# Optimization experiments

Hardware: AMD Instinct MI355X
Metric: run time of the kernel (lower is better)

Reference implementation:

```python
import jax, jax.numpy as jnp
import numpy as np

N = 100000
E = 1600000
NFEAT, NHID, NCLASS = 128, 64, 40
EPS = 1e-5


def _sage_conv(x, src, dst, wl, wr, b):
    # mean aggregation over in-neighbors: out[dst] = mean_{src->dst} x[src]
    msg = jax.ops.segment_sum(x[src], dst, num_segments=N)          # [N, d]
    deg = jax.ops.segment_sum(jnp.ones((src.shape[0],), x.dtype), dst, num_segments=N)
    agg = msg / jnp.maximum(deg, 1.0)[:, None]
    return agg @ wl + x @ wr + b


def _bn_eval(x, g, b, m, v):
    return (x - m) * (g * jax.lax.rsqrt(v + EPS)) + b


def setup_inputs() -> dict:
    key = jax.random.key(0)
    ks = jax.random.split(key, 12)
    s = 0.05
    x = jax.random.normal(ks[0], (N, NFEAT), dtype=jnp.float32)
    edge_index = jax.random.randint(ks[1], (2, E), 0, N, dtype=jnp.int64)
    inp = {
        'x': x,
        'edge_index': edge_index,
        'w1l': jax.random.normal(ks[2], (NFEAT, NHID), jnp.float32) * s,
        'w1r': jax.random.normal(ks[3], (NFEAT, NHID), jnp.float32) * s,
        'b1': jnp.zeros((NHID,), jnp.float32),
        'wxl': jax.random.normal(ks[4], (NHID, NHID), jnp.float32) * s,
        'wxr': jax.random.normal(ks[5], (NHID, NHID), jnp.float32) * s,
        'bx': jnp.zeros((NHID,), jnp.float32),
        'w2l': jax.random.normal(ks[6], (NHID, NCLASS), jnp.float32) * s,
        'w2r': jax.random.normal(ks[7], (NHID, NCLASS), jnp.float32) * s,
        'b2': jnp.zeros((NCLASS,), jnp.float32),
        'bn3_g': jnp.ones((NHID,), jnp.float32),
        'bn3_b': jnp.zeros((NHID,), jnp.float32),
        'bn3_m': jax.random.normal(ks[8], (NHID,), jnp.float32) * 0.1,
        'bn3_v': jax.random.uniform(ks[9], (NHID,), jnp.float32, 0.5, 1.5),
        'bn2_g': jnp.ones((NCLASS,), jnp.float32),
        'bn2_b': jnp.zeros((NCLASS,), jnp.float32),
        'bn2_m': jax.random.normal(ks[10], (NCLASS,), jnp.float32) * 0.1,
        'bn2_v': jax.random.uniform(ks[11], (NCLASS,), jnp.float32, 0.5, 1.5),
    }
    return inp


def reference(x, edge_index, w1l, w1r, b1, wxl, wxr, bx, w2l, w2r, b2,
              bn3_g, bn3_b, bn3_m, bn3_v, bn2_g, bn2_b, bn2_m, bn2_v):
    src, dst = edge_index[0], edge_index[1]
    h = jax.nn.relu(_sage_conv(x, src, dst, w1l, w1r, b1))          # conv1 + relu
    # middle layer (layer=3 -> one convx iteration); dropout = identity (eval)
    h = _sage_conv(h, src, dst, wxl, wxr, bx)
    h = jax.nn.relu(_bn_eval(h, bn3_g, bn3_b, bn3_m, bn3_v))
    # final layer
    h = _sage_conv(h, src, dst, w2l, w2r, b2)
    return _bn_eval(h, bn2_g, bn2_b, bn2_m, bn2_v)                  # [N, NCLASS]
```

## Files before the change

kernel.cpp:

```cpp
#include <hip/hip_runtime.h>

#define NNODES 100000
#define NEDGES 1600000
#define NBK    196
#define BK_CAP 9000
#define CHUNK  4096

typedef short bhalf8 __attribute__((ext_vector_type(8)));
typedef float f32x4 __attribute__((ext_vector_type(4)));

__device__ __forceinline__ unsigned fbits(float x){ union{float f;unsigned u;}c; c.f=x; return c.u; }
__device__ __forceinline__ float bcast(unsigned u){ union{float f;unsigned u;}c; c.u=u; return c.f; }
__device__ __forceinline__ unsigned short rtn16(float x){
    unsigned u = fbits(x);
    return (unsigned short)((u + 0x7FFFu + ((u >> 16) & 1u)) >> 16);
}
__device__ __forceinline__ float b2f(unsigned short b){ return bcast((unsigned)b << 16); }

__global__ void detect_kernel(const int* __restrict__ ei, int* __restrict__ flag) {
    int t = threadIdx.x;
    int v = ei[2 * t + 1];
    unsigned long long nz = __ballot(v != 0);
    if (t == 0) flag[0] = (nz == 0ULL) ? 1 : 0;
}

__global__ __launch_bounds__(256) void bucketize(
    const int* __restrict__ ei, const int* __restrict__ flag,
    unsigned* __restrict__ recs, int* __restrict__ bcur) {
    const int is64 = flag[0];
    __shared__ int cnt[256], base[256], loc[256], rnk[256];
    __shared__ unsigned stage[CHUNK];
    __shared__ unsigned char bkof[CHUNK];
    const int t = threadIdx.x;
    const long start = (long)blockIdx.x * CHUNK;
    cnt[t] = 0; rnk[t] = 0;
    __syncthreads();
#pragma unroll
    for (int k = 0; k < CHUNK / 256; ++k) {
        long e = start + k * 256 + t;
        if (e < NEDGES) {
            int d = is64 ? ei[2 * (NEDGES + e)] : ei[NEDGES + e];
            atomicAdd(&cnt[d >> 9], 1);
        }
    }
    __syncthreads();
    int v = cnt[t];
    int run = v;
    loc[t] = run;
    __syncthreads();
    for (int off = 1; off < 256; off <<= 1) {
        int other = (t >= off) ? loc[t - off] : 0;
        __syncthreads();
        run += other;
        loc[t] = run;
        __syncthreads();
    }
    int excl = run - v;
    if (v > 0) base[t] = atomicAdd(&bcur[t], v);
    loc[t] = excl;
    __syncthreads();
#pragma unroll
    for (int k = 0; k < CHUNK / 256; ++k) {
        long e = start + k * 256 + t;
        if (e < NEDGES) {
            int s = is64 ? ei[2 * e] : ei[e];
            int d = is64 ? ei[2 * (NEDGES + e)] : ei[NEDGES + e];
            int b = d >> 9;
            int r = atomicAdd(&rnk[b], 1);
            int pos = loc[b] + r;
            stage[pos] = ((unsigned)s << 9) | (unsigned)(d & 511);
            bkof[pos] = (unsigned char)b;
        }
    }
    __syncthreads();
    const int tot = (int)min((long)CHUNK, NEDGES - start);
    for (int i = t; i < tot; i += 256) {
        int b = bkof[i];
        int pos = base[b] + (i - loc[b]);
        if (pos < BK_CAP)
            recs[(size_t)b * BK_CAP + pos] = stage[i];
    }
}

__global__ __launch_bounds__(512) void csr_build(
    const unsigned* __restrict__ recs, const int* __restrict__ bcur,
    int* __restrict__ offs, int* __restrict__ csr) {
    const int b = blockIdx.x;
    const int t = threadIdx.x;
    const int lo = b << 9;
    __shared__ int sc[512];
    __shared__ int hist[512];
    __shared__ int loff[512];
    int bv = (t < NBK) ? bcur[t] : 0;
    int run = bv;
    sc[t] = run;
    __syncthreads();
    for (int off = 1; off < 512; off <<= 1) {
        int other = (t >= off) ? sc[t - off] : 0;
        __syncthreads();
        run += other;
        sc[t] = run;
        __syncthreads();
    }
    const int n = bcur[b];
    const int csr_base = sc[b] - n;
    const unsigned* P = recs + (size_t)b * BK_CAP;
    hist[t] = 0;
    __syncthreads();
    for (int i = t; i < n; i += 512)
        atomicAdd(&hist[P[i] & 511], 1);
    __syncthreads();
    int hv = hist[t];
    int hrun = hv;
    sc[t] = hrun;
    __syncthreads();
    for (int off = 1; off < 512; off <<= 1) {
        int other = (t >= off) ? sc[t - off] : 0;
        __syncthreads();
        hrun += other;
        sc[t] = hrun;
        __syncthreads();
    }
    int ex = hrun - hv;
    loff[t] = ex;
    int node = lo + t;
    if (node < NNODES) offs[node] = csr_base + ex;
    if (b == NBK - 1 && t == 0) offs[NNODES] = NEDGES;
    __syncthreads();
    hist[t] = loff[t];
    __syncthreads();
    for (int i = t; i < n; i += 512) {
        unsigned rec = P[i];
        int r = atomicAdd(&hist[rec & 511], 1);
        csr[csr_base + r] = (int)(rec >> 9) * 128;
    }
}

template <int K, int NL, int NTOT>
__global__ void prep_w(const float* __restrict__ wl, const float* __restrict__ wr,
                       const float* __restrict__ bias,
                       const float* __restrict__ g, const float* __restrict__ bb,
                       const float* __restrict__ m, const float* __restrict__ vv,
                       unsigned short* __restrict__ Bh, unsigned short* __restrict__ Bl,
                       float* __restrict__ bfix) {
    constexpr int NCT = NTOT / 16;
    constexpr int TOT = (K / 32) * NCT * 512;
    int tid = blockIdx.x * blockDim.x + threadIdx.x;
    if (tid < NL) {
        float sc = g ? g[tid] * rsqrtf(vv[tid] + 1e-5f) : 1.f;
        float sh = g ? (bb[tid] - m[tid] * sc) : 0.f;
        bfix[tid] = bias[tid] * sc + sh;
    }
    for (int idx = tid; idx < TOT; idx += gridDim.x * blockDim.x) {
        int e = idx & 7, l = (idx >> 3) & 63, rest = idx >> 9;
        int ct = rest % NCT, kc = rest / NCT;
        int k = kc * 32 + (l >> 4) * 8 + e;
        int j = ct * 16 + (l & 15);
        int jj = (j < NL) ? j : j - NL;
        float sc = g ? g[jj] * rsqrtf(vv[jj] + 1e-5f) : 1.f;
        float v = ((j < NL) ? wl[k * NL + j] : wr[k * NL + (j - NL)]) * sc;
        unsigned short h = rtn16(v);
        float r1 = v - bcast((unsigned)h << 16);
        Bh[idx] = h;
        Bl[idx] = rtn16(r1);
    }
}

template <int K, int NL, int NTOT, bool ABF16>
__global__ __launch_bounds__(256) void gemm_mfma(
    const void* __restrict__ hvp, const unsigned short* __restrict__ Bh,
    const unsigned short* __restrict__ Bl, const float* __restrict__ bias,
    unsigned short* __restrict__ zl, unsigned short* __restrict__ zr, int nrows) {
    constexpr int NCT = NTOT / 16;
    constexpr int NKC = K / 32;
    int t = threadIdx.x;
    int l = t & 63, w = t >> 6;
    int rb = blockIdx.x * 64 + w * 16;
    int arow = rb + (l & 15);
    int kg = l >> 4;
    f32x4 acc[NCT];
#pragma unroll
    for (int ct = 0; ct < NCT; ++ct) acc[ct] = (f32x4){0.f, 0.f, 0.f, 0.f};
    const bool aok = (arow < nrows);
#pragma unroll
    for (int kc = 0; kc < NKC; ++kc) {
        bhalf8 ah = {0,0,0,0,0,0,0,0}, al = {0,0,0,0,0,0,0,0};
        if (ABF16) {
            const unsigned short* hr =
                (const unsigned short*)hvp + (long)arow * K + kg * 8;
            if (aok) ah = *(const bhalf8*)(hr + kc * 32);
        } else {
            const float* hr = (const float*)hvp + (long)arow * K + kg * 8;
            float4 a0 = make_float4(0.f, 0.f, 0.f, 0.f), a1 = a0;
            if (aok) {
                a0 = *(const float4*)(hr + kc * 32);
                a1 = *(const float4*)(hr + kc * 32 + 4);
            }
            float av[8] = {a0.x, a0.y, a0.z, a0.w, a1.x, a1.y, a1.z, a1.w};
#pragma unroll
            for (int e = 0; e < 8; ++e) {
                unsigned short hh = rtn16(av[e]);
                float r1 = av[e] - bcast((unsigned)hh << 16);
                ah[e] = (short)hh;
                al[e] = (short)rtn16(r1);
            }
        }
        const unsigned short* hp = Bh + (size_t)(kc * NCT) * 512 + l * 8;
        const unsigned short* lp = Bl + (size_t)(kc * NCT) * 512 + l * 8;
#pragma unroll
        for (int ct = 0; ct < NCT; ++ct) {
            bhalf8 bh = *(const bhalf8*)(hp + ct * 512);
            bhalf8 bl = *(const bhalf8*)(lp + ct * 512);
            acc[ct] = __builtin_amdgcn_mfma_f32_16x16x32_bf16(ah, bh, acc[ct], 0, 0, 0);
            acc[ct] = __builtin_amdgcn_mfma_f32_16x16x32_bf16(ah, bl, acc[ct], 0, 0, 0);
            if (!ABF16)
                acc[ct] = __builtin_amdgcn_mfma_f32_16x16x32_bf16(al, bh, acc[ct], 0, 0, 0);
        }
    }
    int orow0 = rb + kg * 4;
#pragma unroll
    for (int ct = 0; ct < NCT; ++ct) {
        int j = ct * 16 + (l & 15);
        bool isl = (j < NL);
        int cc = isl ? j : j - NL;
        float bj = isl ? 0.f : bias[cc];
#pragma unroll
        for (int r = 0; r < 4; ++r) {
            int orow = orow0 + r;
            if (orow < nrows) {
                if (isl) zl[(long)orow * 64 + cc] = rtn16(acc[ct][r]);
                else     zr[(long)orow * NL + cc] = rtn16(acc[ct][r] + bj);
            }
        }
    }
}

template <int NOUT, bool RELU, typename OUTT>
__global__ __launch_bounds__(256) void combine_kernel(
    const unsigned short* __restrict__ zl, const unsigned short* __restrict__ zr,
    const int* __restrict__ offs, const int* __restrict__ csr,
    OUTT* __restrict__ out) {
    int wid  = (blockIdx.x * blockDim.x + threadIdx.x) >> 6;
    int lane = threadIdx.x & 63;
    if (wid >= NNODES) return;
    int q    = lane >> 5;
    int li2  = (lane & 31) * 2;
    int lib  = li2 * 2;
    constexpr bool FULL = (NOUT == 64);
    const bool cok = FULL || (li2 < NOUT);
    const char* zlb = (const char*)zl;
    float zr0 = 0.f, zr1 = 0.f;
    if (cok) {
        unsigned u = *(const unsigned*)&zr[(long)wid * NOUT + li2];
        zr0 = bcast(u << 16); zr1 = bcast(u & 0xFFFF0000u);
    }
    int s0 = offs[wid], s1 = offs[wid + 1];
    float ax = 0.f, ay = 0.f;
    for (int base = s0; base < s1; base += 64) {
        int c = min(64, s1 - base);
        int cm1 = c - 1;
        int sv = (base + lane < s1) ? csr[base + lane] : 0;
        for (int p0 = 0; p0 < c; p0 += 16) {
            unsigned hv[8];
            if (p0 + 16 <= c) {
#pragma unroll
                for (int j = 0; j < 8; ++j) {
                    int soff = __shfl(sv, p0 + 2 * j + q);
                    unsigned tv = 0;
                    if (cok) tv = *(const unsigned*)(zlb + soff + lib);
                    hv[j] = tv;
                }
            } else {
#pragma unroll
                for (int j = 0; j < 8; ++j) {
                    int eidx = p0 + 2 * j + q;
                    int soff = __shfl(sv, min(eidx, cm1));
                    unsigned tv = 0;
                    if (eidx < c && cok)
                        tv = *(const unsigned*)(zlb + soff + lib);
                    hv[j] = tv;
                }
            }
#pragma unroll
            for (int j = 0; j < 8; ++j) {
                ax += bcast(hv[j] << 16);
                ay += bcast(hv[j] & 0xFFFF0000u);
            }
        }
    }
    ax += __shfl_xor(ax, 32);
    ay += __shfl_xor(ay, 32);
    if (q != 0 || !cok) return;
    float invd = 1.f / fmaxf((float)(s1 - s0), 1.f);
    float r0 = ax * invd + zr0;
    float r1 = ay * invd + zr1;
    if (RELU) { r0 = fmaxf(r0, 0.f); r1 = fmaxf(r1, 0.f); }
    if constexpr (sizeof(OUTT) == 4) {
        *(float2*)&out[(long)wid * NOUT + li2] = make_float2(r0, r1);
    } else {
        *(ushort2*)&out[(long)wid * NOUT + li2] = make_ushort2(rtn16(r0), rtn16(r1));
    }
}

extern "C" void kernel_launch(void* const* d_in, const int* in_sizes, int n_in,
                              void* d_out, int out_size, void* d_ws, size_t ws_size,
                              hipStream_t stream) {
    const float* x    = (const float*)d_in[0];
    const int*   ei   = (const int*)d_in[1];
    const float* w1l  = (const float*)d_in[2];
    const float* w1r  = (const float*)d_in[3];
    const float* b1   = (const float*)d_in[4];
    const float* wxl  = (const float*)d_in[5];
    const float* wxr  = (const float*)d_in[6];
    const float* bx   = (const float*)d_in[7];
    const float* w2l  = (const float*)d_in[8];
    const float* w2r  = (const float*)d_in[9];
    const float* b2   = (const float*)d_in[10];
    const float* bn3g = (const float*)d_in[11];
    const float* bn3b = (const float*)d_in[12];
    const float* bn3m = (const float*)d_in[13];
    const float* bn3v = (const float*)d_in[14];
    const float* bn2g = (const float*)d_in[15];
    const float* bn2b = (const float*)d_in[16];
    const float* bn2m = (const float*)d_in[17];
    const float* bn2v = (const float*)d_in[18];
    float* out = (float*)d_out;

    char* p = (char*)d_ws;
    auto alloc = [&](size_t bytes) -> void* {
        void* r = (void*)p;
        p += (bytes + 255) & ~(size_t)255;
        return r;
    };
    int*   flag   = (int*)alloc(4);
    int*   bcur   = (int*)alloc(NBK * 4);
    int*   offs   = (int*)alloc((size_t)(NNODES + 1) * 4);
    int*   csr    = (int*)alloc((size_t)NEDGES * 4);
    unsigned short* h16  = (unsigned short*)alloc((size_t)NNODES * 64 * 2);
    unsigned short* zl16 = (unsigned short*)alloc((size_t)NNODES * 64 * 2);
    unsigned short* zr16 = (unsigned short*)alloc((size_t)NNODES * 64 * 2);
    unsigned short* B1h = (unsigned short*)alloc(16384 * 2);
    unsigned short* B1l = (unsigned short*)alloc(16384 * 2);
    unsigned short* B2h = (unsigned short*)alloc(8192 * 2);
    unsigned short* B2l = (unsigned short*)alloc(8192 * 2);
    unsigned short* B3h = (unsigned short*)alloc(5120 * 2);
    unsigned short* B3l = (unsigned short*)alloc(5120 * 2);
    float* bfix1 = (float*)alloc(64 * 4);
    float* bfix2 = (float*)alloc(64 * 4);
    float* bfix3 = (float*)alloc(40 * 4);
    unsigned* recs = (unsigned*)h16;

    hipMemsetAsync(bcur, 0, NBK * 4, stream);
    detect_kernel<<<1, 64, 0, stream>>>(ei, flag);
    bucketize<<<(NEDGES + CHUNK - 1) / CHUNK, 256, 0, stream>>>(ei, flag, recs, bcur);
    prep_w<128, 64, 128><<<64, 256, 0, stream>>>(w1l, w1r, b1, nullptr, nullptr, nullptr, nullptr, B1h, B1l, bfix1);
    prep_w<64, 64, 128><<<32, 256, 0, stream>>>(wxl, wxr, bx, bn3g, bn3b, bn3m, bn3v, B2h, B2l, bfix2);
    prep_w<64, 40, 80><<<20, 256, 0, stream>>>(w2l, w2r, b2, bn2g, bn2b, bn2m, bn2v, B3h, B3l, bfix3);
    csr_build<<<NBK, 512, 0, stream>>>(recs, bcur, offs, csr);

    const int GB = (NNODES + 63) / 64;
    gemm_mfma<128, 64, 128, false><<<GB, 256, 0, stream>>>(x, B1h, B1l, bfix1, zl16, zr16, NNODES);
    combine_kernel<64, true, unsigned short><<<25000, 256, 0, stream>>>(
        zl16, zr16, offs, csr, h16);
    gemm_mfma<64, 64, 128, true><<<GB, 256, 0, stream>>>(h16, B2h, B2l, bfix2, zl16, zr16, NNODES);
    combine_kernel<64, true, unsigned short><<<25000, 256, 0, stream>>>(
        zl16, zr16, offs, csr, h16);
    gemm_mfma<64, 40, 80, true><<<GB, 256, 0, stream>>>(h16, B3h, B3l, bfix3, zl16, zr16, NNODES);
    combine_kernel<40, false, float><<<25000, 256, 0, stream>>>(
        zl16, zr16, offs, csr, out);
}
```

Baseline: 226.7 us.

## Pad CSR neighbor lists to multiples of 16 with zero-row sentinel, merge setup kernels

Each node's neighbor list is padded to a multiple of 16 entries. The padding points at an extra all-zero row appended to zl, so the gather loop in combine needs no tail branches or bounds checks. The CSR now stores start/end pairs plus a separate degree array, and one histogram/scan pass in csr_build replaces two. The format-detect kernel is folded into bucketize and the three weight-prep launches are merged into one, cutting launch count. In exchange the padded entries add extra gather loads, and the CSR uses a fixed per-bucket capacity that assumes bounded degrees.

```diff
diff --git a/kernel.cpp b/kernel.cpp
--- a/kernel.cpp
+++ b/kernel.cpp
@@ -4,7 +4,9 @@
 #define NEDGES 1600000
 #define NBK    196
 #define BK_CAP 9000
+#define BKP    17024
 #define CHUNK  4096
+#define ZOFF   (NNODES * 128)
 
 typedef short bhalf8 __attribute__((ext_vector_type(8)));
 typedef float f32x4 __attribute__((ext_vector_type(4)));
@@ -15,31 +17,29 @@
     unsigned u = fbits(x);
     return (unsigned short)((u + 0x7FFFu + ((u >> 16) & 1u)) >> 16);
 }
-__device__ __forceinline__ float b2f(unsigned short b){ return bcast((unsigned)b << 16); }
-
-__global__ void detect_kernel(const int* __restrict__ ei, int* __restrict__ flag) {
-    int t = threadIdx.x;
-    int v = ei[2 * t + 1];
-    unsigned long long nz = __ballot(v != 0);
-    if (t == 0) flag[0] = (nz == 0ULL) ? 1 : 0;
-}
 
 __global__ __launch_bounds__(256) void bucketize(
-    const int* __restrict__ ei, const int* __restrict__ flag,
-    unsigned* __restrict__ recs, int* __restrict__ bcur) {
-    const int is64 = flag[0];
+    const int* __restrict__ ei, unsigned* __restrict__ recs, int* __restrict__ bcur) {
+    __shared__ int s_is64;
     __shared__ int cnt[256], base[256], loc[256], rnk[256];
     __shared__ unsigned stage[CHUNK];
     __shared__ unsigned char bkof[CHUNK];
     const int t = threadIdx.x;
+    if (t < 64) {
+        int v = ei[2 * t + 1];
+        unsigned long long nz = __ballot(v != 0);
+        if (t == 0) s_is64 = (nz == 0ULL) ? 1 : 0;
+    }
+    cnt[t] = 0; rnk[t] = 0;
+    __syncthreads();
+    const int is64 = s_is64;
     const long start = (long)blockIdx.x * CHUNK;
-    cnt[t] = 0; rnk[t] = 0;
-    __syncthreads();
+    const int2* ei2 = (const int2*)ei;
 #pragma unroll
     for (int k = 0; k < CHUNK / 256; ++k) {
         long e = start + k * 256 + t;
         if (e < NEDGES) {
-            int d = is64 ? ei[2 * (NEDGES + e)] : ei[NEDGES + e];
+            int d = is64 ? ei2[NEDGES + e].x : ei[NEDGES + e];
             atomicAdd(&cnt[d >> 9], 1);
         }
     }
@@ -63,8 +63,8 @@
     for (int k = 0; k < CHUNK / 256; ++k) {
         long e = start + k * 256 + t;
         if (e < NEDGES) {
-            int s = is64 ? ei[2 * e] : ei[e];
-            int d = is64 ? ei[2 * (NEDGES + e)] : ei[NEDGES + e];
+            int s = is64 ? ei2[e].x : ei[e];
+            int d = is64 ? ei2[NEDGES + e].x : ei[NEDGES + e];
             int b = d >> 9;
             int r = atomicAdd(&rnk[b], 1);
             int pos = loc[b] + r;
@@ -84,15 +84,23 @@
 
 __global__ __launch_bounds__(512) void csr_build(
     const unsigned* __restrict__ recs, const int* __restrict__ bcur,
-    int* __restrict__ offs, int* __restrict__ csr) {
+    int2* __restrict__ offs2, int* __restrict__ degs, int* __restrict__ csr) {
     const int b = blockIdx.x;
     const int t = threadIdx.x;
     const int lo = b << 9;
     __shared__ int sc[512];
     __shared__ int hist[512];
-    __shared__ int loff[512];
-    int bv = (t < NBK) ? bcur[t] : 0;
-    int run = bv;
+    __shared__ int lstart[512];
+    const int n = bcur[b];
+    const unsigned* P = recs + (size_t)b * BK_CAP;
+    hist[t] = 0;
+    __syncthreads();
+    for (int i = t; i < n; i += 512)
+        atomicAdd(&hist[P[i] & 511], 1);
+    __syncthreads();
+    const int deg = hist[t];
+    const int pad = (deg + 15) & ~15;
+    int run = pad;
     sc[t] = run;
     __syncthreads();
     for (int off = 1; off < 512; off <<= 1) {
@@ -102,56 +110,40 @@
         sc[t] = run;
         __syncthreads();
     }
-    const int n = bcur[b];
-    const int csr_base = sc[b] - n;
-    const unsigned* P = recs + (size_t)b * BK_CAP;
+    const int start = b * BKP + (run - pad);
+    lstart[t] = start;
+    const int node = lo + t;
+    if (node < NNODES) {
+        offs2[node] = make_int2(start, start + pad);
+        degs[node] = deg;
+    }
     hist[t] = 0;
-    __syncthreads();
-    for (int i = t; i < n; i += 512)
-        atomicAdd(&hist[P[i] & 511], 1);
-    __syncthreads();
-    int hv = hist[t];
-    int hrun = hv;
-    sc[t] = hrun;
-    __syncthreads();
-    for (int off = 1; off < 512; off <<= 1) {
-        int other = (t >= off) ? sc[t - off] : 0;
-        __syncthreads();
-        hrun += other;
-        sc[t] = hrun;
-        __syncthreads();
-    }
-    int ex = hrun - hv;
-    loff[t] = ex;
-    int node = lo + t;
-    if (node < NNODES) offs[node] = csr_base + ex;
-    if (b == NBK - 1 && t == 0) offs[NNODES] = NEDGES;
-    __syncthreads();
-    hist[t] = loff[t];
     __syncthreads();
     for (int i = t; i < n; i += 512) {
         unsigned rec = P[i];
-        int r = atomicAdd(&hist[rec & 511], 1);
-        csr[csr_base + r] = (int)(rec >> 9) * 128;
-    }
+        int d = rec & 511;
+        int r = atomicAdd(&hist[d], 1);
+        csr[lstart[d] + r] = (int)(rec >> 9) * 128;
+    }
+    __syncthreads();
+    for (int i = deg; i < pad; ++i)
+        csr[start + i] = ZOFF;
 }
 
 template <int K, int NL, int NTOT>
-__global__ void prep_w(const float* __restrict__ wl, const float* __restrict__ wr,
-                       const float* __restrict__ bias,
-                       const float* __restrict__ g, const float* __restrict__ bb,
-                       const float* __restrict__ m, const float* __restrict__ vv,
-                       unsigned short* __restrict__ Bh, unsigned short* __restrict__ Bl,
-                       float* __restrict__ bfix) {
+__device__ __forceinline__ void prep_section(
+    int blk, int nblk, const float* wl, const float* wr, const float* bias,
+    const float* g, const float* bb, const float* m, const float* vv,
+    unsigned short* Bh, unsigned short* Bl, float* bfix) {
     constexpr int NCT = NTOT / 16;
     constexpr int TOT = (K / 32) * NCT * 512;
-    int tid = blockIdx.x * blockDim.x + threadIdx.x;
+    int tid = blk * 256 + threadIdx.x;
     if (tid < NL) {
         float sc = g ? g[tid] * rsqrtf(vv[tid] + 1e-5f) : 1.f;
         float sh = g ? (bb[tid] - m[tid] * sc) : 0.f;
         bfix[tid] = bias[tid] * sc + sh;
     }
-    for (int idx = tid; idx < TOT; idx += gridDim.x * blockDim.x) {
+    for (int idx = tid; idx < TOT; idx += nblk * 256) {
         int e = idx & 7, l = (idx >> 3) & 63, rest = idx >> 9;
         int ct = rest % NCT, kc = rest / NCT;
         int k = kc * 32 + (l >> 4) * 8 + e;
@@ -164,6 +156,27 @@
         Bh[idx] = h;
         Bl[idx] = rtn16(r1);
     }
+}
+
+__global__ __launch_bounds__(256) void prep_all(
+    const float* w1l, const float* w1r, const float* b1,
+    const float* wxl, const float* wxr, const float* bx,
+    const float* w2l, const float* w2r, const float* b2,
+    const float* g3, const float* bb3, const float* m3, const float* v3,
+    const float* g2, const float* bb2, const float* m2, const float* v2,
+    unsigned short* B1h, unsigned short* B1l, float* bf1,
+    unsigned short* B2h, unsigned short* B2l, float* bf2,
+    unsigned short* B3h, unsigned short* B3l, float* bf3) {
+    int blk = blockIdx.x;
+    if (blk < 64)
+        prep_section<128, 64, 128>(blk, 64, w1l, w1r, b1,
+                                   nullptr, nullptr, nullptr, nullptr, B1h, B1l, bf1);
+    else if (blk < 96)
+        prep_section<64, 64, 128>(blk - 64, 32, wxl, wxr, bx,
+                                  g3, bb3, m3, v3, B2h, B2l, bf2);
+    else
+        prep_section<64, 40, 80>(blk - 96, 20, w2l, w2r, b2,
+                                 g2, bb2, m2, v2, B3h, B3l, bf3);
 }
 
 template <int K, int NL, int NTOT, bool ABF16>
@@ -230,6 +243,8 @@
             if (orow < nrows) {
                 if (isl) zl[(long)orow * 64 + cc] = rtn16(acc[ct][r]);
                 else     zr[(long)orow * NL + cc] = rtn16(acc[ct][r] + bj);
+            } else if (orow == nrows && isl) {
+                zl[(long)orow * 64 + cc] = 0;
             }
         }
     }
@@ -238,48 +253,29 @@
 template <int NOUT, bool RELU, typename OUTT>
 __global__ __launch_bounds__(256) void combine_kernel(
     const unsigned short* __restrict__ zl, const unsigned short* __restrict__ zr,
-    const int* __restrict__ offs, const int* __restrict__ csr,
-    OUTT* __restrict__ out) {
+    const int2* __restrict__ offs2, const int* __restrict__ degs,
+    const int* __restrict__ csr, OUTT* __restrict__ out) {
     int wid  = (blockIdx.x * blockDim.x + threadIdx.x) >> 6;
     int lane = threadIdx.x & 63;
     if (wid >= NNODES) return;
     int q    = lane >> 5;
     int li2  = (lane & 31) * 2;
-    int lib  = li2 * 2;
-    constexpr bool FULL = (NOUT == 64);
-    const bool cok = FULL || (li2 < NOUT);
+    unsigned lib = (unsigned)li2 * 2;
     const char* zlb = (const char*)zl;
-    float zr0 = 0.f, zr1 = 0.f;
-    if (cok) {
-        unsigned u = *(const unsigned*)&zr[(long)wid * NOUT + li2];
-        zr0 = bcast(u << 16); zr1 = bcast(u & 0xFFFF0000u);
-    }
-    int s0 = offs[wid], s1 = offs[wid + 1];
+    unsigned uzr = *(const unsigned*)&zr[(long)wid * NOUT + li2];
+    float zr0 = bcast(uzr << 16), zr1 = bcast(uzr & 0xFFFF0000u);
+    float invd = 1.f / fmaxf((float)degs[wid], 1.f);
+    int2 se = offs2[wid];
     float ax = 0.f, ay = 0.f;
-    for (int base = s0; base < s1; base += 64) {
-        int c = min(64, s1 - base);
-        int cm1 = c - 1;
-        int sv = (base + lane < s1) ? csr[base + lane] : 0;
+    for (int base = se.x; base < se.y; base += 64) {
+        int c = min(64, se.y - base);
+        int sv = csr[base + lane];
         for (int p0 = 0; p0 < c; p0 += 16) {
             unsigned hv[8];
-            if (p0 + 16 <= c) {
-#pragma unroll
-                for (int j = 0; j < 8; ++j) {
-                    int soff = __shfl(sv, p0 + 2 * j + q);
-                    unsigned tv = 0;
-                    if (cok) tv = *(const unsigned*)(zlb + soff + lib);
-                    hv[j] = tv;
-                }
-            } else {
-#pragma unroll
-                for (int j = 0; j < 8; ++j) {
-                    int eidx = p0 + 2 * j + q;
-                    int soff = __shfl(sv, min(eidx, cm1));
-                    unsigned tv = 0;
-                    if (eidx < c && cok)
-                        tv = *(const unsigned*)(zlb + soff + lib);
-                    hv[j] = tv;
-                }
+#pragma unroll
+            for (int j = 0; j < 8; ++j) {
+                unsigned soff = (unsigned)__shfl(sv, p0 + 2 * j + q);
+                hv[j] = *(const unsigned*)(zlb + soff + lib);
             }
 #pragma unroll
             for (int j = 0; j < 8; ++j) {
@@ -290,8 +286,7 @@
     }
     ax += __shfl_xor(ax, 32);
     ay += __shfl_xor(ay, 32);
-    if (q != 0 || !cok) return;
-    float invd = 1.f / fmaxf((float)(s1 - s0), 1.f);
+    if (q != 0 || li2 >= NOUT) return;
     float r0 = ax * invd + zr0;
     float r1 = ay * invd + zr1;
     if (RELU) { r0 = fmaxf(r0, 0.f); r1 = fmaxf(r1, 0.f); }
@@ -332,12 +327,12 @@
         p += (bytes + 255) & ~(size_t)255;
         return r;
     };
-    int*   flag   = (int*)alloc(4);
-    int*   bcur   = (int*)alloc(NBK * 4);
-    int*   offs   = (int*)alloc((size_t)(NNODES + 1) * 4);
-    int*   csr    = (int*)alloc((size_t)NEDGES * 4);
+    int*   bcur  = (int*)alloc(NBK * 4);
+    int2*  offs2 = (int2*)alloc((size_t)NNODES * 8);
+    int*   degs  = (int*)alloc((size_t)NNODES * 4);
+    int*   csr   = (int*)alloc(((size_t)NBK * BKP + 64) * 4);
     unsigned short* h16  = (unsigned short*)alloc((size_t)NNODES * 64 * 2);
-    unsigned short* zl16 = (unsigned short*)alloc((size_t)NNODES * 64 * 2);
+    unsigned short* zl16 = (unsigned short*)alloc((size_t)(NNODES + 1) * 64 * 2);
     unsigned short* zr16 = (unsigned short*)alloc((size_t)NNODES * 64 * 2);
     unsigned short* B1h = (unsigned short*)alloc(16384 * 2);
     unsigned short* B1l = (unsigned short*)alloc(16384 * 2);
@@ -351,21 +346,20 @@
     unsigned* recs = (unsigned*)h16;
 
     hipMemsetAsync(bcur, 0, NBK * 4, stream);
-    detect_kernel<<<1, 64, 0, stream>>>(ei, flag);
-    bucketize<<<(NEDGES + CHUNK - 1) / CHUNK, 256, 0, stream>>>(ei, flag, recs, bcur);
-    prep_w<128, 64, 128><<<64, 256, 0, stream>>>(w1l, w1r, b1, nullptr, nullptr, nullptr, nullptr, B1h, B1l, bfix1);
-    prep_w<64, 64, 128><<<32, 256, 0, stream>>>(wxl, wxr, bx, bn3g, bn3b, bn3m, bn3v, B2h, B2l, bfix2);
-    prep_w<64, 40, 80><<<20, 256, 0, stream>>>(w2l, w2r, b2, bn2g, bn2b, bn2m, bn2v, B3h, B3l, bfix3);
-    csr_build<<<NBK, 512, 0, stream>>>(recs, bcur, offs, csr);
+    bucketize<<<(NEDGES + CHUNK - 1) / CHUNK, 256, 0, stream>>>(ei, recs, bcur);
+    prep_all<<<116, 256, 0, stream>>>(w1l, w1r, b1, wxl, wxr, bx, w2l, w2r, b2,
+                                      bn3g, bn3b, bn3m, bn3v, bn2g, bn2b, bn2m, bn2v,
+                                      B1h, B1l, bfix1, B2h, B2l, bfix2, B3h, B3l, bfix3);
+    csr_build<<<NBK, 512, 0, stream>>>(recs, bcur, offs2, degs, csr);
 
     const int GB = (NNODES + 63) / 64;
     gemm_mfma<128, 64, 128, false><<<GB, 256, 0, stream>>>(x, B1h, B1l, bfix1, zl16, zr16, NNODES);
     combine_kernel<64, true, unsigned short><<<25000, 256, 0, stream>>>(
-        zl16, zr16, offs, csr, h16);
+        zl16, zr16, offs2, degs, csr, h16);
     gemm_mfma<64, 64, 128, true><<<GB, 256, 0, stream>>>(h16, B2h, B2l, bfix2, zl16, zr16, NNODES);
     combine_kernel<64, true, unsigned short><<<25000, 256, 0, stream>>>(
-        zl16, zr16, offs, csr, h16);
+        zl16, zr16, offs2, degs, csr, h16);
     gemm_mfma<64, 40, 80, true><<<GB, 256, 0, stream>>>(h16, B3h, B3l, bfix3, zl16, zr16, NNODES);
     combine_kernel<40, false, float><<<25000, 256, 0, stream>>>(
-        zl16, zr16, offs, csr, out);
-}
+        zl16, zr16, offs2, degs, csr, out);
+}
```

Measured after the change: 220.5 us. 1.03x faster.
